# Optimization experiments

Measured on AMD Instinct MI355X. Metric: run time of the kernel, lower is better.

## Reference

```python
import jax, jax.numpy as jnp
import numpy as np

B, S, D = 64, 500, 1024  # batch, seq_len, input_dim == hidden_dim
MAX_POS = 500

def _lin(k, din, dout):
    k1, k2 = jax.random.split(k)
    s = 1.0 / np.sqrt(din)
    W = jax.random.uniform(k1, (din, dout), jnp.float32, -s, s)
    b = jax.random.uniform(k2, (dout,), jnp.float32, -s, s)
    return W, b

def setup_inputs() -> dict:
    key = jax.random.key(0)
    ks = jax.random.split(key, 12)
    x = jax.random.normal(ks[0], (B, S, D), jnp.float32)
    pos_emb = jax.random.normal(ks[1], (MAX_POS, D), jnp.float32)
    Wq_fw, bq_fw = _lin(ks[2], D, D)
    Wk_fw, bk_fw = _lin(ks[3], D, D)
    Wv_fw, bv_fw = _lin(ks[4], D, D)
    Wq_bw, bq_bw = _lin(ks[5], D, D)
    Wk_bw, bk_bw = _lin(ks[6], D, D)
    Wv_bw, bv_bw = _lin(ks[7], D, D)
    Wg_fw, bg_fw = _lin(ks[8], 2 * D, D)
    Wg_bw, bg_bw = _lin(ks[9], 2 * D, D)
    W2, b2 = _lin(ks[10], 2 * D, 2 * D)
    W1, b1 = _lin(ks[11], 2 * D, 2 * D)
    return dict(x=x, pos_emb=pos_emb,
                Wq_fw=Wq_fw, bq_fw=bq_fw, Wk_fw=Wk_fw, bk_fw=bk_fw, Wv_fw=Wv_fw, bv_fw=bv_fw,
                Wq_bw=Wq_bw, bq_bw=bq_bw, Wk_bw=Wk_bw, bk_bw=bk_bw, Wv_bw=Wv_bw, bv_bw=bv_bw,
                Wg_fw=Wg_fw, bg_fw=bg_fw, Wg_bw=Wg_bw, bg_bw=bg_bw,
                W2=W2, b2=b2, W1=W1, b1=b1)

def _attn(q, k, v, mask, d):
    # q,k,v: [B,S,D]; mask: [S,S] bool (True = keep)
    scores = jnp.einsum('bqd,bkd->bqk', q, k) / jnp.sqrt(jnp.float32(d))
    scores = jnp.where(mask[None], scores, jnp.float32(-1e9))
    probs = jax.nn.softmax(scores, axis=-1)  # dropout is identity in eval
    return jnp.einsum('bqk,bkd->bqd', probs, v)

def reference(x, pos_emb, Wq_fw, bq_fw, Wk_fw, bk_fw, Wv_fw, bv_fw,
              Wq_bw, bq_bw, Wk_bw, bk_bw, Wv_bw, bv_bw,
              Wg_fw, bg_fw, Wg_bw, bg_bw, W2, b2, W1, b1):
    b, s, d = x.shape
    H = x + pos_emb[:s][None]  # [B,S,D]
    tri = jnp.tril(jnp.ones((s, s), dtype=bool))
    H_mF = _attn(H @ Wq_fw + bq_fw, H @ Wk_fw + bk_fw, H @ Wv_fw + bv_fw, tri, d)
    H_mB = _attn(H @ Wq_bw + bq_bw, H @ Wk_bw + bk_bw, H @ Wv_bw + bv_bw, tri.T, d)
    G_fw = jax.nn.sigmoid(jnp.concatenate([H, H_mF], -1) @ Wg_fw + bg_fw)
    C_F = G_fw * H + (1.0 - G_fw) * H_mF
    G_bw = jax.nn.sigmoid(jnp.concatenate([H, H_mB], -1) @ Wg_bw + bg_bw)
    C_B = G_bw * H + (1.0 - G_bw) * H_mB
    C_i = jnp.concatenate([C_F, C_B], -1)  # [B,S,2D]
    activ = jax.nn.sigmoid(C_i @ W2 + b2)
    scores = activ @ W1 + b1
    attn_w = jax.nn.softmax(scores, axis=1)  # softmax over seq dim
    utt_vec = jnp.sum(attn_w * C_i, axis=1)  # [B,2D]
    return utt_vec, C_i
```

## Files before the change

### kernel.cpp

```cpp
#include <hip/hip_runtime.h>

typedef __bf16 bf16;
typedef __bf16 bf16x4 __attribute__((ext_vector_type(4)));
typedef __bf16 bf16x8 __attribute__((ext_vector_type(8)));
typedef float  f32x4  __attribute__((ext_vector_type(4)));
typedef unsigned int u32;

#define GLD_LDS16(gsrc, ldst) \
  __builtin_amdgcn_global_load_lds((const __attribute__((address_space(1))) u32*)(gsrc), \
                                   (__attribute__((address_space(3))) u32*)(ldst), 16, 0, 0)

static __device__ __forceinline__ float sigmoidf_(float x) { return 1.0f / (1.0f + expf(-x)); }

__global__ void fill_guard(float* __restrict__ utt, float v) {
  int i = blockIdx.x * 256 + threadIdx.x;
  if (i < 131072) utt[i] = v;
}

__global__ void add_pos_bf(const float* __restrict__ x, const float* __restrict__ pos,
                           bf16* __restrict__ H) {
  size_t i = ((size_t)blockIdx.x * 256 + threadIdx.x) * 4;
  if (i >= 32768000ull) return;
  int d = (int)(i & 1023);
  int s = (int)((i >> 10) % 500);
  float4 xv = *(const float4*)(x + i);
  float4 pv = *(const float4*)(pos + (size_t)s * 1024 + d);
  bf16x4 o;
  o[0] = (bf16)(xv.x + pv.x); o[1] = (bf16)(xv.y + pv.y);
  o[2] = (bf16)(xv.z + pv.z); o[3] = (bf16)(xv.w + pv.w);
  *(bf16x4*)(H + i) = o;
}

__global__ void wtrans(const float* __restrict__ src, bf16* __restrict__ dst, int R, int C) {
  __shared__ float tile[32][33];
  int c0 = blockIdx.x * 32, r0 = blockIdx.y * 32;
  int tr = threadIdx.x >> 5, tc = threadIdx.x & 31;
#pragma unroll
  for (int i = 0; i < 4; ++i)
    tile[tr + i * 8][tc] = src[(size_t)(r0 + tr + i * 8) * C + c0 + tc];
  __syncthreads();
#pragma unroll
  for (int i = 0; i < 4; ++i) {
    int rr = tr + i * 8;
    dst[(size_t)(c0 + rr) * R + r0 + tc] = (bf16)tile[tc][rr];
  }
}

__global__ void ci2bf(const float* __restrict__ src, bf16* __restrict__ dst) {
  size_t i = ((size_t)blockIdx.x * 256 + threadIdx.x) * 4;
  if (i >= 65536000ull) return;
  float4 v = *(const float4*)(src + i);
  bf16x4 o;
  o[0] = (bf16)v.x; o[1] = (bf16)v.y; o[2] = (bf16)v.z; o[3] = (bf16)v.w;
  *(bf16x4*)(dst + i) = o;
}

template <int EPI, typename TC>
__global__ __launch_bounds__(256, 2) void mgemm(
    const bf16* __restrict__ A, const bf16* __restrict__ A2, int ksplit,
    const bf16* __restrict__ Bt, const float* __restrict__ bias, TC* __restrict__ C,
    int M, int N, int K, int lda, int ldb, int ldc, int c_off, float scale,
    long long sA, long long sB, long long sC,
    const bf16* __restrict__ Gh, const bf16* __restrict__ Gm) {
  __shared__ __align__(16) char sm[16384];
  const int t = threadIdx.x;
  const long long bz = blockIdx.z;
  A += bz * sA; A2 += bz * sA; Bt += bz * sB; C += bz * sC;
  const int m0 = blockIdx.y * 128, n0 = blockIdx.x * 128;

  f32x4 acc[4][4];
#pragma unroll
  for (int i = 0; i < 4; ++i)
#pragma unroll
    for (int j = 0; j < 4; ++j)
#pragma unroll
      for (int c = 0; c < 4; ++c) acc[i][j][c] = 0.0f;

  const int lane = t & 63;
  const int wv = t >> 6, wm = (wv >> 1) * 64, wn = (wv & 1) * 64;
  const int lr = lane & 15, lkb = (lane >> 4) * 16;
  const int rr = t >> 2, cc = (t & 3) * 8;

  for (int k0 = 0; k0 < K; k0 += 32) {
    const bf16* Ak = (k0 < ksplit) ? (A + k0) : (A2 + (k0 - ksplit));
    const bf16* Bk = Bt + k0;
#pragma unroll
    for (int j = 0; j < 2; ++j) {
      int ra = m0 + j * 64 + rr; ra = ra < M ? ra : M - 1;
      GLD_LDS16(Ak + (size_t)ra * lda + cc, sm + j * 4096 + t * 16);
      int rb = n0 + j * 64 + rr; rb = rb < N ? rb : N - 1;
      GLD_LDS16(Bk + (size_t)rb * ldb + cc, sm + 8192 + j * 4096 + t * 16);
    }
    asm volatile("s_waitcnt vmcnt(0)" ::: "memory");
    __syncthreads();

    bf16x8 av[4], bv[4];
#pragma unroll
    for (int i = 0; i < 4; ++i) {
      av[i] = *(const bf16x8*)(sm + (wm + i * 16 + lr) * 64 + lkb);
      bv[i] = *(const bf16x8*)(sm + 8192 + (wn + i * 16 + lr) * 64 + lkb);
    }
#pragma unroll
    for (int i = 0; i < 4; ++i)
#pragma unroll
      for (int j = 0; j < 4; ++j)
        acc[i][j] = __builtin_amdgcn_mfma_f32_16x16x32_bf16(av[i], bv[j], acc[i][j], 0, 0, 0);
    __syncthreads();
  }

#pragma unroll
  for (int i = 0; i < 4; ++i) {
#pragma unroll
    for (int j4 = 0; j4 < 4; ++j4) {
      int m = m0 + wm + i * 16 + (lane >> 4) * 4 + j4;
      if (m >= M) continue;
#pragma unroll
      for (int j = 0; j < 4; ++j) {
        int n = n0 + wn + j * 16 + (lane & 15);
        if (n >= N) continue;
        float v = acc[i][j][j4] * scale;
        if (bias) v += bias[n];
        if (EPI == 1) v = sigmoidf_(v);
        if (EPI == 2) {
          float g = sigmoidf_(v);
          float h  = (float)Gh[(size_t)m * 1024 + n];
          float hm = (float)Gm[(size_t)m * 1024 + n];
          v = g * h + (1.0f - g) * hm;
        }
        if (EPI == 3) {
          unsigned b = (unsigned)m / 500u;
          unsigned s = (unsigned)m - b * 500u;
          C[(size_t)b * 524288 + (size_t)n * 512 + s] = (TC)v;
        } else {
          C[(size_t)m * ldc + c_off + n] = (TC)v;
        }
      }
    }
  }
}

__global__ void attn_softmax_w(const float* __restrict__ S, bf16* __restrict__ P, int fw) {
  int row = blockIdx.x * 4 + (threadIdx.x >> 6);
  int lane = threadIdx.x & 63;
  int q = row % 500;
  const float* Srow = S + (size_t)row * 512;
  bf16* Prow = P + (size_t)row * 512;
  int klo = fw ? 0 : q;
  int khi = fw ? q : 499;

  float xv[8];
  float m = -1e30f;
#pragma unroll
  for (int i = 0; i < 8; ++i) {
    int k = lane + i * 64;
    bool valid = (k >= klo) & (k <= khi);
    float v = valid ? Srow[k] : -1e30f;
    xv[i] = v;
    m = fmaxf(m, v);
  }
#pragma unroll
  for (int off = 32; off > 0; off >>= 1) m = fmaxf(m, __shfl_xor(m, off, 64));
  float e[8];
  float sum = 0.0f;
#pragma unroll
  for (int i = 0; i < 8; ++i) {
    e[i] = (xv[i] > -1e29f) ? expf(xv[i] - m) : 0.0f;
    sum += e[i];
  }
#pragma unroll
  for (int off = 32; off > 0; off >>= 1) sum += __shfl_xor(sum, off, 64);
  float inv = 1.0f / sum;
#pragma unroll
  for (int i = 0; i < 8; ++i) Prow[lane + i * 64] = (bf16)(e[i] * inv);
}

__global__ void final_reduce_chunk(const float* __restrict__ s2, const float* __restrict__ Ci,
                                   float* __restrict__ utt) {
  int c = blockIdx.x * 256 + threadIdx.x;
  int b = blockIdx.y;
  if (c >= 2048) return;
  float m = -1e30f;
  for (int s = 0; s < 500; ++s) m = fmaxf(m, s2[((size_t)(b * 500 + s)) * 2048 + c]);
  float sum = 0.0f, acc = 0.0f;
  for (int s = 0; s < 500; ++s) {
    size_t idx = ((size_t)(b * 500 + s)) * 2048 + c;
    float e = expf(s2[idx] - m);
    sum += e;
    acc += e * Ci[idx];
  }
  utt[(size_t)b * 2048 + c] = acc / sum;
}

extern "C" void kernel_launch(void* const* d_in, const int* in_sizes, int n_in,
                              void* d_out, int out_size, void* d_ws, size_t ws_size,
                              hipStream_t stream) {
  (void)in_sizes; (void)n_in; (void)out_size;
  float* utt = (float*)d_out;
  float* Ci  = (float*)d_out + 131072;

  const float* x     = (const float*)d_in[0];
  const float* pos   = (const float*)d_in[1];
  const float* Wq_fw = (const float*)d_in[2];  const float* bq_fw = (const float*)d_in[3];
  const float* Wk_fw = (const float*)d_in[4];  const float* bk_fw = (const float*)d_in[5];
  const float* Wv_fw = (const float*)d_in[6];  const float* bv_fw = (const float*)d_in[7];
  const float* Wq_bw = (const float*)d_in[8];  const float* bq_bw = (const float*)d_in[9];
  const float* Wk_bw = (const float*)d_in[10]; const float* bk_bw = (const float*)d_in[11];
  const float* Wv_bw = (const float*)d_in[12]; const float* bv_bw = (const float*)d_in[13];
  const float* Wg_fw = (const float*)d_in[14]; const float* bg_fw = (const float*)d_in[15];
  const float* Wg_bw = (const float*)d_in[16]; const float* bg_bw = (const float*)d_in[17];
  const float* W2    = (const float*)d_in[18]; const float* b2    = (const float*)d_in[19];
  const float* W1    = (const float*)d_in[20]; const float* b1    = (const float*)d_in[21];

  const size_t WS_BYTES = 399769600ull;
  if (ws_size < WS_BYTES) { fill_guard<<<512, 256, 0, stream>>>(utt, 500.0f); return; }

  char* wsb = (char*)d_ws;
  bf16*  Hbf  = (bf16*)(wsb);
  bf16*  Qb   = (bf16*)(wsb + 65536000);
  bf16*  Kb   = (bf16*)(wsb + 131072000);
  bf16*  Vt   = (bf16*)(wsb + 196608000);
  float* Sb   = (float*)(wsb + 263716864);
  bf16*  Hmb  = (bf16*)(wsb + 263716864);
  bf16*  Pb   = (bf16*)(wsb + 329252864);
  char*  wts  = wsb + 362020864;
  bf16* WqF = (bf16*)(wts);             bf16* WkF = (bf16*)(wts + 2097152);
  bf16* WvF = (bf16*)(wts + 4194304);   bf16* WqB = (bf16*)(wts + 6291456);
  bf16* WkB = (bf16*)(wts + 8388608);   bf16* WvB = (bf16*)(wts + 10485760);
  bf16* WgF = (bf16*)(wts + 12582912);  bf16* WgB = (bf16*)(wts + 16777216);
  bf16* W2t = (bf16*)(wts + 20971520);  bf16* W1t = (bf16*)(wts + 29360128);
  bf16*  Cibf  = (bf16*)(wsb);
  bf16*  activ = (bf16*)(wsb + 131072000);
  float* s2b   = (float*)(wsb);

  add_pos_bf<<<32000, 256, 0, stream>>>(x, pos, Hbf);

  struct WT { const float* s; bf16* d; int R, C; } wt[10] = {
      {Wq_fw, WqF, 1024, 1024}, {Wk_fw, WkF, 1024, 1024}, {Wv_fw, WvF, 1024, 1024},
      {Wq_bw, WqB, 1024, 1024}, {Wk_bw, WkB, 1024, 1024}, {Wv_bw, WvB, 1024, 1024},
      {Wg_fw, WgF, 2048, 1024}, {Wg_bw, WgB, 2048, 1024},
      {W2,    W2t, 2048, 2048}, {W1,    W1t, 2048, 2048}};
  for (int i = 0; i < 10; ++i)
    wtrans<<<dim3(wt[i].C / 32, wt[i].R / 32), 256, 0, stream>>>(wt[i].s, wt[i].d, wt[i].R, wt[i].C);

  const int BIG = 1 << 30;
  for (int dir = 0; dir < 2; ++dir) {
    const bf16* WqT = dir ? WqB : WqF;  const float* bq = dir ? bq_bw : bq_fw;
    const bf16* WkT = dir ? WkB : WkF;  const float* bk = dir ? bk_bw : bk_fw;
    const bf16* WvT = dir ? WvB : WvF;  const float* bv = dir ? bv_bw : bv_fw;
    const bf16* WgT = dir ? WgB : WgF;  const float* bg = dir ? bg_bw : bg_fw;

    mgemm<0, bf16><<<dim3(8, 250, 1), 256, 0, stream>>>(
        Hbf, Hbf, BIG, WqT, bq, Qb, 32000, 1024, 1024, 1024, 1024, 1024, 0, 1.0f,
        0, 0, 0, nullptr, nullptr);
    mgemm<0, bf16><<<dim3(8, 250, 1), 256, 0, stream>>>(
        Hbf, Hbf, BIG, WkT, bk, Kb, 32000, 1024, 1024, 1024, 1024, 1024, 0, 1.0f,
        0, 0, 0, nullptr, nullptr);
    mgemm<3, bf16><<<dim3(8, 250, 1), 256, 0, stream>>>(
        Hbf, Hbf, BIG, WvT, bv, Vt, 32000, 1024, 1024, 1024, 1024, 512, 0, 1.0f,
        0, 0, 0, nullptr, nullptr);
    mgemm<0, float><<<dim3(4, 4, 64), 256, 0, stream>>>(
        Qb, Qb, BIG, Kb, nullptr, Sb, 500, 500, 1024, 1024, 1024, 512, 0, 0.03125f,
        512000, 512000, 256000, nullptr, nullptr);
    attn_softmax_w<<<8000, 256, 0, stream>>>(Sb, Pb, dir == 0 ? 1 : 0);
    mgemm<0, bf16><<<dim3(8, 4, 64), 256, 0, stream>>>(
        Pb, Pb, BIG, Vt, nullptr, Hmb, 500, 1024, 512, 512, 512, 1024, 0, 1.0f,
        256000, 524288, 512000, nullptr, nullptr);
    mgemm<2, float><<<dim3(8, 250, 1), 256, 0, stream>>>(
        Hbf, Hmb, 1024, WgT, bg, Ci, 32000, 1024, 2048, 1024, 2048, 2048,
        dir == 0 ? 0 : 1024, 1.0f, 0, 0, 0, Hbf, Hmb);
  }

  ci2bf<<<64000, 256, 0, stream>>>(Ci, Cibf);

  mgemm<1, bf16><<<dim3(16, 250, 1), 256, 0, stream>>>(
      Cibf, Cibf, BIG, W2t, b2, activ, 32000, 2048, 2048, 2048, 2048, 2048, 0, 1.0f,
      0, 0, 0, nullptr, nullptr);

  for (int c0 = 0; c0 < 2; ++c0) {
    mgemm<0, float><<<dim3(16, 125, 1), 256, 0, stream>>>(
        activ + (size_t)c0 * 16000 * 2048, activ, BIG, W1t, b1, s2b,
        16000, 2048, 2048, 2048, 2048, 2048, 0, 1.0f, 0, 0, 0, nullptr, nullptr);
    final_reduce_chunk<<<dim3(8, 32), 256, 0, stream>>>(
        s2b, Ci + (size_t)c0 * 32 * 500 * 2048, utt + (size_t)c0 * 32 * 2048);
  }
}
```

Before: 2.884 ms.

## Fuse bf16 Ci copy into gate GEMM, remap workgroups per XCD, online softmax reduce

The gate GEMM epilogue now also writes a bf16 copy of C_i into a new workspace region, so the separate float-to-bf16 conversion pass over the whole C_i tensor is removed. The GEMM maps block IDs so that consecutive tiles land on the same XCD, aiming for better L2 reuse on the multi-die MI355X. The final reduction uses a single-pass online softmax instead of two passes over s2, which saves one full read at the cost of an extra exp per element. The workspace requirement grows by about 64 MB.

```diff
diff --git a/kernel.cpp b/kernel.cpp
--- a/kernel.cpp
+++ b/kernel.cpp
@@ -46,19 +46,11 @@
   }
 }
 
-__global__ void ci2bf(const float* __restrict__ src, bf16* __restrict__ dst) {
-  size_t i = ((size_t)blockIdx.x * 256 + threadIdx.x) * 4;
-  if (i >= 65536000ull) return;
-  float4 v = *(const float4*)(src + i);
-  bf16x4 o;
-  o[0] = (bf16)v.x; o[1] = (bf16)v.y; o[2] = (bf16)v.z; o[3] = (bf16)v.w;
-  *(bf16x4*)(dst + i) = o;
-}
-
 template <int EPI, typename TC>
 __global__ __launch_bounds__(256, 2) void mgemm(
     const bf16* __restrict__ A, const bf16* __restrict__ A2, int ksplit,
     const bf16* __restrict__ Bt, const float* __restrict__ bias, TC* __restrict__ C,
+    bf16* __restrict__ Cbf,
     int M, int N, int K, int lda, int ldb, int ldc, int c_off, float scale,
     long long sA, long long sB, long long sC,
     const bf16* __restrict__ Gh, const bf16* __restrict__ Gm) {
@@ -66,7 +58,14 @@
   const int t = threadIdx.x;
   const long long bz = blockIdx.z;
   A += bz * sA; A2 += bz * sA; Bt += bz * sB; C += bz * sC;
-  const int m0 = blockIdx.y * 128, n0 = blockIdx.x * 128;
+
+  const int gx = gridDim.x;
+  const int nwg = gx * gridDim.y;
+  const int orig = blockIdx.y * gx + blockIdx.x;
+  const int qq = nwg >> 3, r8 = nwg & 7;
+  const int xcd = orig & 7, lo = orig >> 3;
+  const int wg = (xcd < r8 ? xcd * (qq + 1) : r8 * (qq + 1) + (xcd - r8) * qq) + lo;
+  const int m0 = (wg / gx) * 128, n0 = (wg % gx) * 128;
 
   f32x4 acc[4][4];
 #pragma unroll
@@ -133,6 +132,7 @@
           C[(size_t)b * 524288 + (size_t)n * 512 + s] = (TC)v;
         } else {
           C[(size_t)m * ldc + c_off + n] = (TC)v;
+          if (EPI == 2 && Cbf) Cbf[(size_t)m * 2048 + c_off + n] = (bf16)v;
         }
       }
     }
@@ -179,14 +179,17 @@
   int c = blockIdx.x * 256 + threadIdx.x;
   int b = blockIdx.y;
   if (c >= 2048) return;
-  float m = -1e30f;
-  for (int s = 0; s < 500; ++s) m = fmaxf(m, s2[((size_t)(b * 500 + s)) * 2048 + c]);
-  float sum = 0.0f, acc = 0.0f;
+  float m = -1e30f, sum = 0.0f, acc = 0.0f;
   for (int s = 0; s < 500; ++s) {
     size_t idx = ((size_t)(b * 500 + s)) * 2048 + c;
-    float e = expf(s2[idx] - m);
-    sum += e;
-    acc += e * Ci[idx];
+    float xx = s2[idx];
+    float ci = Ci[idx];
+    float mn = fmaxf(m, xx);
+    float corr = expf(m - mn);
+    float e = expf(xx - mn);
+    sum = sum * corr + e;
+    acc = acc * corr + e * ci;
+    m = mn;
   }
   utt[(size_t)b * 2048 + c] = acc / sum;
 }
@@ -211,7 +214,7 @@
   const float* W2    = (const float*)d_in[18]; const float* b2    = (const float*)d_in[19];
   const float* W1    = (const float*)d_in[20]; const float* b1    = (const float*)d_in[21];
 
-  const size_t WS_BYTES = 399769600ull;
+  const size_t WS_BYTES = 465305600ull;
   if (ws_size < WS_BYTES) { fill_guard<<<512, 256, 0, stream>>>(utt, 500.0f); return; }
 
   char* wsb = (char*)d_ws;
@@ -228,7 +231,7 @@
   bf16* WkB = (bf16*)(wts + 8388608);   bf16* WvB = (bf16*)(wts + 10485760);
   bf16* WgF = (bf16*)(wts + 12582912);  bf16* WgB = (bf16*)(wts + 16777216);
   bf16* W2t = (bf16*)(wts + 20971520);  bf16* W1t = (bf16*)(wts + 29360128);
-  bf16*  Cibf  = (bf16*)(wsb);
+  bf16*  Cibf  = (bf16*)(wsb + 399769600);
   bf16*  activ = (bf16*)(wsb + 131072000);
   float* s2b   = (float*)(wsb);
 
@@ -250,35 +253,33 @@
     const bf16* WgT = dir ? WgB : WgF;  const float* bg = dir ? bg_bw : bg_fw;
 
     mgemm<0, bf16><<<dim3(8, 250, 1), 256, 0, stream>>>(
-        Hbf, Hbf, BIG, WqT, bq, Qb, 32000, 1024, 1024, 1024, 1024, 1024, 0, 1.0f,
+        Hbf, Hbf, BIG, WqT, bq, Qb, nullptr, 32000, 1024, 1024, 1024, 1024, 1024, 0, 1.0f,
         0, 0, 0, nullptr, nullptr);
     mgemm<0, bf16><<<dim3(8, 250, 1), 256, 0, stream>>>(
-        Hbf, Hbf, BIG, WkT, bk, Kb, 32000, 1024, 1024, 1024, 1024, 1024, 0, 1.0f,
+        Hbf, Hbf, BIG, WkT, bk, Kb, nullptr, 32000, 1024, 1024, 1024, 1024, 1024, 0, 1.0f,
         0, 0, 0, nullptr, nullptr);
     mgemm<3, bf16><<<dim3(8, 250, 1), 256, 0, stream>>>(
-        Hbf, Hbf, BIG, WvT, bv, Vt, 32000, 1024, 1024, 1024, 1024, 512, 0, 1.0f,
+        Hbf, Hbf, BIG, WvT, bv, Vt, nullptr, 32000, 1024, 1024, 1024, 1024, 512, 0, 1.0f,
         0, 0, 0, nullptr, nullptr);
     mgemm<0, float><<<dim3(4, 4, 64), 256, 0, stream>>>(
-        Qb, Qb, BIG, Kb, nullptr, Sb, 500, 500, 1024, 1024, 1024, 512, 0, 0.03125f,
+        Qb, Qb, BIG, Kb, nullptr, Sb, nullptr, 500, 500, 1024, 1024, 1024, 512, 0, 0.03125f,
         512000, 512000, 256000, nullptr, nullptr);
     attn_softmax_w<<<8000, 256, 0, stream>>>(Sb, Pb, dir == 0 ? 1 : 0);
     mgemm<0, bf16><<<dim3(8, 4, 64), 256, 0, stream>>>(
-        Pb, Pb, BIG, Vt, nullptr, Hmb, 500, 1024, 512, 512, 512, 1024, 0, 1.0f,
+        Pb, Pb, BIG, Vt, nullptr, Hmb, nullptr, 500, 1024, 512, 512, 512, 1024, 0, 1.0f,
         256000, 524288, 512000, nullptr, nullptr);
     mgemm<2, float><<<dim3(8, 250, 1), 256, 0, stream>>>(
-        Hbf, Hmb, 1024, WgT, bg, Ci, 32000, 1024, 2048, 1024, 2048, 2048,
+        Hbf, Hmb, 1024, WgT, bg, Ci, Cibf, 32000, 1024, 2048, 1024, 2048, 2048,
         dir == 0 ? 0 : 1024, 1.0f, 0, 0, 0, Hbf, Hmb);
   }
 
-  ci2bf<<<64000, 256, 0, stream>>>(Ci, Cibf);
-
   mgemm<1, bf16><<<dim3(16, 250, 1), 256, 0, stream>>>(
-      Cibf, Cibf, BIG, W2t, b2, activ, 32000, 2048, 2048, 2048, 2048, 2048, 0, 1.0f,
+      Cibf, Cibf, BIG, W2t, b2, activ, nullptr, 32000, 2048, 2048, 2048, 2048, 2048, 0, 1.0f,
       0, 0, 0, nullptr, nullptr);
 
   for (int c0 = 0; c0 < 2; ++c0) {
     mgemm<0, float><<<dim3(16, 125, 1), 256, 0, stream>>>(
-        activ + (size_t)c0 * 16000 * 2048, activ, BIG, W1t, b1, s2b,
+        activ + (size_t)c0 * 16000 * 2048, activ, BIG, W1t, b1, s2b, nullptr,
         16000, 2048, 2048, 2048, 2048, 2048, 0, 1.0f, 0, 0, 0, nullptr, nullptr);
     final_reduce_chunk<<<dim3(8, 32), 256, 0, stream>>>(
         s2b, Ci + (size_t)c0 * 32 * 500 * 2048, utt + (size_t)c0 * 32 * 2048);
```

Measured after the change: 2.610 ms. 9.5% less time.
